# Optimization experiments

Measured on AMD Instinct MI355X. Metric: run time of the kernel, lower is better.

The kernel has to match this reference:

```python
import jax, jax.numpy as jnp
import numpy as np

B, S, E, C, H = 64, 2048, 512, 512, 256


def setup_inputs() -> dict:
    key = jax.random.key(0)
    ks = jax.random.split(key, 8)
    encoder_word_embeds = jax.random.normal(ks[0], (B, S, E), dtype=jnp.float32)
    encoder_lengths = jax.random.randint(ks[1], (B,), 1, S + 1)  # lengths in [1, S]
    context_state = jax.random.normal(ks[2], (B, C), dtype=jnp.float32)
    # Learned parameters (nn.Linear style: y = x @ W.T + b)
    sw = 1.0 / np.sqrt(E)
    sc = 1.0 / np.sqrt(C)
    sh = 1.0 / np.sqrt(H)
    W_word = jax.random.uniform(ks[3], (H, E), minval=-sw, maxval=sw, dtype=jnp.float32)
    b_word = jax.random.uniform(ks[4], (H,), minval=-sw, maxval=sw, dtype=jnp.float32)
    W_ctx = jax.random.uniform(ks[5], (H, C), minval=-sc, maxval=sc, dtype=jnp.float32)
    b_ctx = jax.random.uniform(ks[6], (H,), minval=-sc, maxval=sc, dtype=jnp.float32)
    w_hidden = jax.random.uniform(ks[7], (H,), minval=-sh, maxval=sh, dtype=jnp.float32)  # hidden_layer has no bias
    return {
        "encoder_word_embeds": encoder_word_embeds,
        "encoder_lengths": encoder_lengths,
        "context_state": context_state,
        "W_word": W_word,
        "b_word": b_word,
        "W_ctx": W_ctx,
        "b_ctx": b_ctx,
        "w_hidden": w_hidden,
    }


def reference(encoder_word_embeds, encoder_lengths, context_state, W_word, b_word, W_ctx, b_ctx, w_hidden):
    seq_len = encoder_word_embeds.shape[1]
    # word mask [B, S]: positions < length
    positions = jnp.arange(seq_len)  # [S]
    mask = (positions[None, :] < encoder_lengths[:, None]).astype(jnp.float32)  # [B, S]
    # additive attention MLP
    word_feat = jnp.einsum("bse,he->bsh", encoder_word_embeds, W_word) + b_word  # [B,S,H]
    ctx_feat = context_state @ W_ctx.T + b_ctx  # [B,H]
    scores = jnp.einsum("bsh,h->bs", jnp.tanh(word_feat + ctx_feat[:, None, :]), w_hidden)  # [B,S]
    # softmax over seq, then mask and renormalize (matches original order)
    attn = jax.nn.softmax(scores, axis=1) * mask
    attn = attn / (1e-10 + attn.sum(axis=1, keepdims=True))  # [B,S]
    attention_features = jnp.einsum("bs,bse->be", attn, encoder_word_embeds)  # [B,E]
    return attention_features, attn
```

## Files before the change

### kernel.cpp

```cpp
#include <hip/hip_runtime.h>
#include <hip/hip_bf16.h>
#include <cstdint>
#include <cstddef>

#define B_  64
#define S_  2048
#define E_  512
#define C_  512
#define H_  256

using f32x4 = __attribute__((ext_vector_type(4))) float;
using s16x8 = __attribute__((ext_vector_type(8))) short;

__device__ __forceinline__ uint2 f4_to_bf4(float4 v) {
    __hip_bfloat162 lo = __float22bfloat162_rn(make_float2(v.x, v.y));
    __hip_bfloat162 hi = __float22bfloat162_rn(make_float2(v.z, v.w));
    union { __hip_bfloat162 b; unsigned u; } a, c;
    a.b = lo; c.b = hi;
    return make_uint2(a.u, c.u);
}

__global__ void prep_w(const float* __restrict__ W, unsigned short* __restrict__ Wb) {
    int i = (blockIdx.x * 256 + threadIdx.x) * 4;
    float4 v = *(const float4*)(W + i);
    uint2 o = f4_to_bf4(v);
    *(uint2*)(Wb + i) = o;
}

__global__ void prep_ctx(const float* __restrict__ ctx, const float* __restrict__ Wc,
                         const float* __restrict__ bc, const float* __restrict__ bw,
                         float* __restrict__ cb) {
    __shared__ float row[C_];
    int b = blockIdx.x, t = threadIdx.x;
    row[t] = ctx[b * C_ + t];
    row[t + 256] = ctx[b * C_ + t + 256];
    __syncthreads();
    const float4* w4 = (const float4*)(Wc + (size_t)t * C_);
    const float4* x4 = (const float4*)row;
    float acc = 0.f;
    #pragma unroll 4
    for (int c = 0; c < C_ / 4; ++c) {
        float4 w = w4[c], x = x4[c];
        acc += w.x * x.x + w.y * x.y + w.z * x.z + w.w * x.w;
    }
    cb[b * H_ + t] = acc + bc[t] + bw[t];
}

#define BM 128
#define BN 256
#define BK 64
#define LDT 72

__global__ __launch_bounds__(512) void scores_kernel(
    const float* __restrict__ A,
    const unsigned short* __restrict__ Wb,
    const float* __restrict__ cb,
    const float* __restrict__ wh,
    const int*   __restrict__ lens,
    float* __restrict__ scores)
{
    __shared__ __align__(16) unsigned short At[BM * LDT];
    __shared__ __align__(16) unsigned short Bt[BN * LDT];
    __shared__ float sblk[BM];
    int t = threadIdx.x;
    int m0 = blockIdx.x * BM;
    int b  = m0 >> 11;
    int ms = m0 & (S_ - 1);
    if (ms >= lens[b]) return;

    int w = t >> 6, lane = t & 63, quad = lane >> 4, lm = lane & 15;
    int wm = (w & 1) * 64, wn = (w >> 1) * 64;

    if (t < BM) sblk[t] = 0.f;

    f32x4 acc[4][4] = {};

    int arow = t >> 4, acol = (t & 15) * 4;
    int brow = t >> 3, bcol = (t & 7) * 8;

    for (int k0 = 0; k0 < E_; k0 += BK) {
        #pragma unroll
        for (int i = 0; i < 4; ++i) {
            int r = arow + i * 32;
            float4 v = *(const float4*)(A + (size_t)(m0 + r) * E_ + k0 + acol);
            *(uint2*)(At + r * LDT + acol) = f4_to_bf4(v);
        }
        #pragma unroll
        for (int i = 0; i < 4; ++i) {
            int r = brow + i * 64;
            uint4 v = *(const uint4*)(Wb + (size_t)r * E_ + k0 + bcol);
            *(uint4*)(Bt + r * LDT + bcol) = v;
        }
        __syncthreads();
        #pragma unroll
        for (int ks = 0; ks < 2; ++ks) {
            s16x8 af[4], bfr[4];
            #pragma unroll
            for (int i = 0; i < 4; ++i)
                af[i] = *(const s16x8*)(At + (wm + i * 16 + lm) * LDT + ks * 32 + quad * 8);
            #pragma unroll
            for (int i = 0; i < 4; ++i)
                bfr[i] = *(const s16x8*)(Bt + (wn + i * 16 + lm) * LDT + ks * 32 + quad * 8);
            #pragma unroll
            for (int mi = 0; mi < 4; ++mi)
                #pragma unroll
                for (int ni = 0; ni < 4; ++ni)
                    acc[mi][ni] = __builtin_amdgcn_mfma_f32_16x16x32_bf16(
                        af[mi], bfr[ni], acc[mi][ni], 0, 0, 0);
        }
        __syncthreads();
    }

    float wv[4], cbv[4];
    #pragma unroll
    for (int ni = 0; ni < 4; ++ni) {
        int n = wn + ni * 16 + lm;
        wv[ni]  = wh[n];
        cbv[ni] = cb[b * H_ + n];
    }
    #pragma unroll
    for (int mi = 0; mi < 4; ++mi) {
        #pragma unroll
        for (int r = 0; r < 4; ++r) {
            float p = 0.f;
            #pragma unroll
            for (int ni = 0; ni < 4; ++ni) {
                float x = acc[mi][ni][r] + cbv[ni];
                x = fminf(fmaxf(x, -15.f), 15.f);
                float e = __expf(2.f * x);
                float th = 1.f - 2.f * __builtin_amdgcn_rcpf(e + 1.f);
                p += wv[ni] * th;
            }
            #pragma unroll
            for (int off = 8; off >= 1; off >>= 1)
                p += __shfl_xor(p, off);
            if (lm == 0)
                atomicAdd(&sblk[wm + mi * 16 + quad * 4 + r], p);
        }
    }
    __syncthreads();
    if (t < BM) scores[m0 + t] = sblk[t];
}

__global__ void softmax_kernel(const int* __restrict__ lens, float* __restrict__ attn) {
    __shared__ float redm[4], redt[4];
    int b = blockIdx.x, t = threadIdx.x;
    int len = lens[b];
    float* sc = attn + (size_t)b * S_;
    float v[8];
    #pragma unroll
    for (int i = 0; i < 8; ++i) {
        int s = t + i * 256;
        v[i] = (s < len) ? sc[s] : -1e30f;
    }
    float m = -1e30f;
    #pragma unroll
    for (int i = 0; i < 8; ++i) m = fmaxf(m, v[i]);
    #pragma unroll
    for (int off = 32; off >= 1; off >>= 1) m = fmaxf(m, __shfl_xor(m, off));
    if ((t & 63) == 0) redm[t >> 6] = m;
    __syncthreads();
    m = fmaxf(fmaxf(redm[0], redm[1]), fmaxf(redm[2], redm[3]));
    float e[8]; float tm = 0.f;
    #pragma unroll
    for (int i = 0; i < 8; ++i) {
        int s = t + i * 256;
        e[i] = (s < len) ? __expf(v[i] - m) : 0.f;
        tm += e[i];
    }
    #pragma unroll
    for (int off = 32; off >= 1; off >>= 1) tm += __shfl_xor(tm, off);
    if ((t & 63) == 0) redt[t >> 6] = tm;
    __syncthreads();
    tm = redt[0] + redt[1] + redt[2] + redt[3];
    float sfac = 1.f / tm;
    #pragma unroll
    for (int i = 0; i < 8; ++i) {
        int s = t + i * 256;
        sc[s] = e[i] * sfac;
    }
}

__global__ __launch_bounds__(512) void wsum_kernel(
    const float* __restrict__ A, const float* __restrict__ attn,
    const int* __restrict__ lens, float* __restrict__ out) {
    int b = blockIdx.y;
    int len = lens[b];
    int s0 = blockIdx.x * 128;
    if (s0 >= len) return;
    int send = s0 + 128; if (send > len) send = len;
    int t  = threadIdx.x;
    int e4 = t & 127;
    int sr = t >> 7;
    const float* ap = attn + (size_t)b * S_;
    f32x4 acc = {0.f, 0.f, 0.f, 0.f};
    const float* base = A + (size_t)b * S_ * E_;
    for (int s = s0 + sr; s < send; s += 4) {
        float wgt = ap[s];
        f32x4 v = *(const f32x4*)(base + (size_t)s * E_ + e4 * 4);
        acc += wgt * v;
    }
    __shared__ f32x4 red[4][128];
    red[sr][e4] = acc;
    __syncthreads();
    if (t < 128) {
        f32x4 tot = red[0][t] + red[1][t] + red[2][t] + red[3][t];
        float* o = out + (size_t)b * E_ + t * 4;
        atomicAdd(o + 0, tot[0]);
        atomicAdd(o + 1, tot[1]);
        atomicAdd(o + 2, tot[2]);
        atomicAdd(o + 3, tot[3]);
    }
}

extern "C" void kernel_launch(void* const* d_in, const int* in_sizes, int n_in,
                              void* d_out, int out_size, void* d_ws, size_t ws_size,
                              hipStream_t stream) {
    const float* embeds = (const float*)d_in[0];
    const int*   lens   = (const int*)d_in[1];
    const float* ctx    = (const float*)d_in[2];
    const float* Ww     = (const float*)d_in[3];
    const float* bw     = (const float*)d_in[4];
    const float* Wc     = (const float*)d_in[5];
    const float* bc     = (const float*)d_in[6];
    const float* wh     = (const float*)d_in[7];
    float* out  = (float*)d_out;
    float* feat = out;
    float* attn = out + B_ * E_;

    unsigned short* Wb = (unsigned short*)d_ws;
    float* cb = (float*)((char*)d_ws + (size_t)H_ * E_ * sizeof(unsigned short));

    hipMemsetAsync(feat, 0, (size_t)B_ * E_ * sizeof(float), stream);
    prep_w<<<(H_ * E_) / 1024, 256, 0, stream>>>(Ww, Wb);
    prep_ctx<<<B_, 256, 0, stream>>>(ctx, Wc, bc, bw, cb);
    scores_kernel<<<dim3(B_ * S_ / BM), 512, 0, stream>>>(embeds, Wb, cb, wh, lens, attn);
    softmax_kernel<<<B_, 256, 0, stream>>>(lens, attn);
    wsum_kernel<<<dim3(S_ / 128, B_), 512, 0, stream>>>(embeds, attn, lens, feat);
}
```

Measured before the change: 428.7 us.

## Load GEMM tiles directly into LDS with async global_load_lds and XOR swizzle

```diff
diff --git a/kernel.cpp b/kernel.cpp
--- a/kernel.cpp
+++ b/kernel.cpp
@@ -18,6 +18,24 @@
     union { __hip_bfloat162 b; unsigned u; } a, c;
     a.b = lo; c.b = hi;
     return make_uint2(a.u, c.u);
+}
+
+__device__ __forceinline__ s16x8 cvt8(f32x4 lo, f32x4 hi) {
+    union { __hip_bfloat162 b; unsigned u; } p0, p1, p2, p3;
+    p0.b = __float22bfloat162_rn(make_float2(lo[0], lo[1]));
+    p1.b = __float22bfloat162_rn(make_float2(lo[2], lo[3]));
+    p2.b = __float22bfloat162_rn(make_float2(hi[0], hi[1]));
+    p3.b = __float22bfloat162_rn(make_float2(hi[2], hi[3]));
+    union { unsigned u[4]; s16x8 s; } r;
+    r.u[0] = p0.u; r.u[1] = p1.u; r.u[2] = p2.u; r.u[3] = p3.u;
+    return r.s;
+}
+
+__device__ __forceinline__ void async16(const void* g, void* l) {
+    __builtin_amdgcn_global_load_lds(
+        (const __attribute__((address_space(1))) void*)g,
+        (__attribute__((address_space(3))) void*)l,
+        16, 0, 0);
 }
 
 __global__ void prep_w(const float* __restrict__ W, unsigned short* __restrict__ Wb) {
@@ -49,7 +67,6 @@
 #define BM 128
 #define BN 256
 #define BK 64
-#define LDT 72
 
 __global__ __launch_bounds__(512) void scores_kernel(
     const float* __restrict__ A,
@@ -59,8 +76,8 @@
     const int*   __restrict__ lens,
     float* __restrict__ scores)
 {
-    __shared__ __align__(16) unsigned short At[BM * LDT];
-    __shared__ __align__(16) unsigned short Bt[BN * LDT];
+    __shared__ __align__(16) float At[BM * 64];
+    __shared__ __align__(16) unsigned short Bt[BN * 64];
     __shared__ float sblk[BM];
     int t = threadIdx.x;
     int m0 = blockIdx.x * BM;
@@ -75,32 +92,44 @@
 
     f32x4 acc[4][4] = {};
 
-    int arow = t >> 4, acol = (t & 15) * 4;
-    int brow = t >> 3, bcol = (t & 7) * 8;
+    int la16 = lane >> 4, lc16 = lane & 15;
+    int la8  = lane >> 3, lc8  = lane & 7;
 
     for (int k0 = 0; k0 < E_; k0 += BK) {
         #pragma unroll
-        for (int i = 0; i < 4; ++i) {
-            int r = arow + i * 32;
-            float4 v = *(const float4*)(A + (size_t)(m0 + r) * E_ + k0 + acol);
-            *(uint2*)(At + r * LDT + acol) = f4_to_bf4(v);
-        }
-        #pragma unroll
-        for (int i = 0; i < 4; ++i) {
-            int r = brow + i * 64;
-            uint4 v = *(const uint4*)(Wb + (size_t)r * E_ + k0 + bcol);
-            *(uint4*)(Bt + r * LDT + bcol) = v;
+        for (int j = 0; j < 4; ++j) {
+            int r  = (w << 4) + (j << 2) + la16;
+            int cg = (lc16 ^ (r & 15)) << 2;
+            async16(A + (size_t)(m0 + r) * E_ + k0 + cg,
+                    (char*)At + (((w << 4) + (j << 2)) << 8));
+        }
+        #pragma unroll
+        for (int j = 0; j < 4; ++j) {
+            int r  = (w << 5) + (j << 3) + la8;
+            int cg = (lc8 ^ (r & 7)) << 3;
+            async16(Wb + (size_t)r * E_ + k0 + cg,
+                    (char*)Bt + (((w << 5) + (j << 3)) << 7));
         }
         __syncthreads();
         #pragma unroll
         for (int ks = 0; ks < 2; ++ks) {
             s16x8 af[4], bfr[4];
             #pragma unroll
-            for (int i = 0; i < 4; ++i)
-                af[i] = *(const s16x8*)(At + (wm + i * 16 + lm) * LDT + ks * 32 + quad * 8);
-            #pragma unroll
-            for (int i = 0; i < 4; ++i)
-                bfr[i] = *(const s16x8*)(Bt + (wn + i * 16 + lm) * LDT + ks * 32 + quad * 8);
+            for (int i = 0; i < 4; ++i) {
+                int r = wm + i * 16 + lm;
+                int x = r & 15;
+                int c0 = (ks * 8 + quad * 2) ^ x;
+                int c1 = (ks * 8 + quad * 2 + 1) ^ x;
+                f32x4 lo = *(const f32x4*)(At + r * 64 + c0 * 4);
+                f32x4 hi = *(const f32x4*)(At + r * 64 + c1 * 4);
+                af[i] = cvt8(lo, hi);
+            }
+            #pragma unroll
+            for (int i = 0; i < 4; ++i) {
+                int r = wn + i * 16 + lm;
+                int c = (ks * 4 + quad) ^ (r & 7);
+                bfr[i] = *(const s16x8*)(Bt + r * 64 + c * 8);
+            }
             #pragma unroll
             for (int mi = 0; mi < 4; ++mi)
                 #pragma unroll
```

Measured after the change: 439.9 us. 1.03x slower.
